# Performance work log

Measured on AMD Instinct MI355X. Metric: run time of the kernel, lower is better.

The kernel has to match this reference:

```python
import jax, jax.numpy as jnp
import numpy as np

BS = 128
HW = 128
REG = 0.1


def setup_inputs() -> dict:
    key = jax.random.key(0)
    k1, k2 = jax.random.split(key)
    x1 = jax.random.normal(k1, (BS, 1, HW, HW), dtype=jnp.float32)
    x2 = jax.random.normal(k2, (BS, 1, HW, HW), dtype=jnp.float32)
    return {"x1": x1, "x2": x2}


def _calc_psd(x):
    # x: [2*bs, H, W]
    dft = jnp.fft.fft2(x)
    avgpsd = jnp.mean((dft * jnp.conj(dft)).real, axis=0)  # [H, W]
    return jnp.mean(jnp.log(avgpsd)) - jnp.log(jnp.mean(avgpsd))


def reference(x1, x2):
    a = x1[:, 0]  # [bs, H, W] (squeeze channel)
    b = x2[:, 0]
    # pairwise Frobenius distances: Dist[i, j] = ||x1[i] - x2[j]||_F
    diff = a[:, None, :, :] - b[None, :, :, :]          # [bs, bs, H, W]
    Dist = jnp.sqrt(jnp.sum(diff * diff, axis=(-2, -1)))  # [bs, bs]
    bs = Dist.shape[0]
    # CrossEntropyLoss(Dist, arange(bs)) = mean_i(logsumexp(Dist[i]) - Dist[i, i])
    log_probs = jax.nn.log_softmax(Dist, axis=-1)
    ce = -jnp.mean(jnp.diagonal(log_probs))
    # PSD regularizer on cat(x1, x2)
    x = jnp.concatenate([a, b], axis=0)  # [2*bs, H, W]
    r = _calc_psd(x)
    return ce - REG * r
```

## Files before the change

### kernel.cpp

```cpp
#include <hip/hip_runtime.h>
#include <math.h>


#define WS_SE    256
#define WS_MX    512
#define WS_DII   768
#define WS_NP    16640
#define WS_GP    20736
#define WS_P     4215040
#define WS_PS    6344960
#define WS_PL    6345025

#define PI_F 3.14159265358979323846f

__device__ __forceinline__ void fft128_reg(float& s0r, float& s0i,
                                           float& s1r, float& s1i,
                                           float cA, float sA,
                                           const float* wr, const float* wi,
                                           int lane) {
    float er = s0r + s1r, ei = s0i + s1i;
    float dr = s0r - s1r, di = s0i - s1i;
    float orr = dr * cA - di * sA;
    float oii = dr * sA + di * cA;
    #pragma unroll
    for (int st = 0; st < 6; ++st) {
        int m = 32 >> st;
        bool up = (lane & m) == 0;
        float tr = __shfl_xor(er, m), ti = __shfl_xor(ei, m);
        float ar = tr - er, ai = ti - ei;
        float e2r = up ? (er + tr) : (ar * wr[st] - ai * wi[st]);
        float e2i = up ? (ei + ti) : (ar * wi[st] + ai * wr[st]);
        tr = __shfl_xor(orr, m); ti = __shfl_xor(oii, m);
        float br_ = tr - orr, bi_ = ti - oii;
        float o2r = up ? (orr + tr) : (br_ * wr[st] - bi_ * wi[st]);
        float o2i = up ? (oii + ti) : (br_ * wi[st] + bi_ * wr[st]);
        er = e2r; ei = e2i; orr = o2r; oii = o2i;
    }
    s0r = er; s0i = ei; s1r = orr; s1i = oii;
}

__global__ __launch_bounds__(512, 4) void ocl_main(const float* __restrict__ x1,
                                                   const float* __restrict__ x2,
                                                   float* __restrict__ ws) {
    __shared__ float4 smem4[4096];
    int t = threadIdx.x;
    int bid = blockIdx.x;

    if (bid < 256) {
        float4* As = smem4;
        float4* Bs = smem4 + 2048;
        int ks = bid, k0q = ks * 16;
        const float4* A = (const float4*)x1;
        const float4* B = (const float4*)x2;
        {
            int qi = t & 15, r0 = t >> 4;
            #pragma unroll
            for (int p = 0; p < 4; ++p) {
                int r = r0 + 32 * p;
                int sq = qi ^ ((r >> 3) & 7);
                As[r * 16 + sq] = A[(size_t)r * 4096 + k0q + qi];
                Bs[r * 16 + sq] = B[(size_t)r * 4096 + k0q + qi];
            }
        }
        __syncthreads();
        if (t >= 256) return;

        int ty = t >> 4, tx = t & 15;
        float acc[8][8];
        #pragma unroll
        for (int r = 0; r < 8; ++r)
            #pragma unroll
            for (int c = 0; c < 8; ++c) acc[r][c] = 0.0f;

        for (int qk = 0; qk < 16; ++qk) {
            int sa = qk ^ (ty & 7);
            int sb = qk ^ (tx & 7);
            float4 a4[8];
            #pragma unroll
            for (int r = 0; r < 8; ++r) a4[r] = As[(ty * 8 + r) * 16 + sa];
            #pragma unroll
            for (int h = 0; h < 2; ++h) {
                float4 b4[4];
                #pragma unroll
                for (int c = 0; c < 4; ++c)
                    b4[c] = Bs[(tx * 8 + h * 4 + c) * 16 + sb];
                #pragma unroll
                for (int r = 0; r < 8; ++r)
                    #pragma unroll
                    for (int c = 0; c < 4; ++c) {
                        float4 a = a4[r], b = b4[c];
                        acc[r][h * 4 + c] = fmaf(a.x, b.x, fmaf(a.y, b.y,
                            fmaf(a.z, b.z, fmaf(a.w, b.w, acc[r][h * 4 + c]))));
                    }
            }
        }

        float4* Gp4 = (float4*)(ws + WS_GP);
        #pragma unroll
        for (int r = 0; r < 8; ++r)
            #pragma unroll
            for (int cc = 0; cc < 2; ++cc) {
                int e4 = (ty * 8 + r) * 32 + tx * 2 + cc;
                Gp4[(size_t)(e4 >> 2) * 1024 + ks * 4 + (e4 & 3)] =
                    make_float4(acc[r][cc * 4 + 0], acc[r][cc * 4 + 1],
                                acc[r][cc * 4 + 2], acc[r][cc * 4 + 3]);
            }
    } else {
        float* zre = (float*)smem4;
        float* zim = zre + 8192;
        int lane = t & 63, wave = t >> 6;
        int img = bid - 256;
        const float* src = (img < 128) ? (x1 + (size_t)img * 16384)
                                       : (x2 + (size_t)(img - 128) * 16384);

        float cA, sA, wr[6], wi[6];
        {
            float th = -PI_F * (float)lane / 64.0f;
            sA = __sinf(th); cA = __cosf(th);
            #pragma unroll
            for (int st = 0; st < 6; ++st) {
                int m = 32 >> st;
                float a = -PI_F * (float)(lane & (m - 1)) / (float)m;
                wi[st] = __sinf(a); wr[st] = __cosf(a);
            }
        }
        int rb = (int)(__brev((unsigned)lane) >> 26);

        float nrm = 0.0f;
        #pragma unroll
        for (int pi = 0; pi < 8; ++pi) {
            int p = wave * 8 + pi;
            const float* r0 = src + p * 256 + lane;
            float s0r = r0[0],   s1r = r0[64];
            float s0i = r0[128], s1i = r0[192];
            nrm += s0r * s0r + s1r * s1r + s0i * s0i + s1i * s1i;
            fft128_reg(s0r, s0i, s1r, s1i, cA, sA, wr, wi, lane);
            int f0 = (2 * rb + p) & 127;
            int f1 = (2 * rb + 1 + p) & 127;
            zre[p * 128 + f0] = s0r; zim[p * 128 + f0] = s0i;
            zre[p * 128 + f1] = s1r; zim[p * 128 + f1] = s1i;
        }
        for (int off = 32; off >= 1; off >>= 1) nrm += __shfl_xor(nrm, off);
        if (lane == 0) ws[WS_NP + img * 8 + wave] = nrm;
        __syncthreads();

        int p0 = (lane >> 1), p1 = 32 + (lane >> 1);
        int par = lane & 1;
        float* P = ws + WS_P;
        for (int k = wave; k < 65; k += 8) {
            float v0r, v0i, v1r, v1i;
            if (k == 0 || k == 64) {
                int c0 = (k + p0) & 127, c1 = (k + p1) & 127;
                float Z0r = zre[p0 * 128 + c0], Z0i = zim[p0 * 128 + c0];
                float Z1r = zre[p1 * 128 + c1], Z1i = zim[p1 * 128 + c1];
                v0r = par ? Z0i : Z0r; v0i = 0.0f;
                v1r = par ? Z1i : Z1r; v1i = 0.0f;
            } else {
                int kn = 128 - k;
                int ck = (k + p0) & 127, cn = (kn + p0) & 127;
                float Zkr = zre[p0 * 128 + ck], Zki = zim[p0 * 128 + ck];
                float Znr = zre[p0 * 128 + cn], Zni = zim[p0 * 128 + cn];
                float e0r = 0.5f * (Zkr + Znr), e0i = 0.5f * (Zki - Zni);
                float q0r = 0.5f * (Zki + Zni), q0i = 0.5f * (Znr - Zkr);
                v0r = par ? q0r : e0r; v0i = par ? q0i : e0i;
                ck = (k + p1) & 127; cn = (kn + p1) & 127;
                Zkr = zre[p1 * 128 + ck]; Zki = zim[p1 * 128 + ck];
                Znr = zre[p1 * 128 + cn]; Zni = zim[p1 * 128 + cn];
                float e1r = 0.5f * (Zkr + Znr), e1i = 0.5f * (Zki - Zni);
                float q1r = 0.5f * (Zki + Zni), q1i = 0.5f * (Znr - Zkr);
                v1r = par ? q1r : e1r; v1i = par ? q1i : e1i;
            }
            fft128_reg(v0r, v0i, v1r, v1i, cA, sA, wr, wi, lane);
            int m = lane & 15, hi = lane >> 4;
            P[(size_t)(k * 8 + 0 + hi) * 4096 + img * 16 + m] = v0r * v0r + v0i * v0i;
            P[(size_t)(k * 8 + 4 + hi) * 4096 + img * 16 + m] = v1r * v1r + v1i * v1i;
        }
    }
}

__global__ __launch_bounds__(256) void ocl_finish(float* __restrict__ ws) {
    int bid = blockIdx.x, t = threadIdx.x;
    int lane = t & 63, wave = t >> 6;

    if (bid < 256) {
        int g = bid;
        const float4* Gp4 = (const float4*)(ws + WS_GP);
        int q = (lane >> 4) & 3, kg = lane & 15;
        const float4* base = Gp4 + (size_t)g * 4096 + wave * 1024 + q;
        float4 v[16];
        #pragma unroll
        for (int it = 0; it < 16; ++it) v[it] = base[(kg * 16 + it) * 4];

        __shared__ float nbs[64];
        __shared__ float s_na;
        __shared__ float sm[4], sm2[4];
        if (t < 64) {
            const float* np = ws + WS_NP + (size_t)(128 + (g & 1) * 64 + t) * 8;
            nbs[t] = ((np[0] + np[1]) + (np[2] + np[3])) +
                     ((np[4] + np[5]) + (np[6] + np[7]));
        }
        if (t == 64) {
            const float* np = ws + WS_NP + (size_t)(g >> 1) * 8;
            s_na = ((np[0] + np[1]) + (np[2] + np[3])) +
                   ((np[4] + np[5]) + (np[6] + np[7]));
        }

        float4 s = v[0];
        #pragma unroll
        for (int it = 1; it < 16; ++it) {
            s.x += v[it].x; s.y += v[it].y; s.z += v[it].z; s.w += v[it].w;
        }
        #pragma unroll
        for (int msk = 1; msk <= 8; msk <<= 1) {
            s.x += __shfl_xor(s.x, msk); s.y += __shfl_xor(s.y, msk);
            s.z += __shfl_xor(s.z, msk); s.w += __shfl_xor(s.w, msk);
        }
        __syncthreads();

        int cq = wave * 4 + q;
        float nai = s_na;
        float4 d;
        d.x = sqrtf(fmaxf(nai + nbs[cq * 4 + 0] - 2.0f * s.x, 0.0f));
        d.y = sqrtf(fmaxf(nai + nbs[cq * 4 + 1] - 2.0f * s.y, 0.0f));
        d.z = sqrtf(fmaxf(nai + nbs[cq * 4 + 2] - 2.0f * s.z, 0.0f));
        d.w = sqrtf(fmaxf(nai + nbs[cq * 4 + 3] - 2.0f * s.w, 0.0f));

        int i = g >> 1;
        int jr = i - (g & 1) * 64;
        if (kg == 0 && jr >= 0 && jr < 64 && cq == (jr >> 2)) {
            float dii = (jr & 2) ? ((jr & 1) ? d.w : d.z) : ((jr & 1) ? d.y : d.x);
            ws[WS_DII + i] = dii;
        }

        float m = fmaxf(fmaxf(d.x, d.y), fmaxf(d.z, d.w));
        m = fmaxf(m, __shfl_xor(m, 16));
        m = fmaxf(m, __shfl_xor(m, 32));
        if (lane == 0) sm[wave] = m;
        __syncthreads();
        float M = fmaxf(fmaxf(sm[0], sm[1]), fmaxf(sm[2], sm[3]));

        float se = __expf(d.x - M) + __expf(d.y - M) +
                   __expf(d.z - M) + __expf(d.w - M);
        se += __shfl_xor(se, 16);
        se += __shfl_xor(se, 32);
        if (lane == 0) sm2[wave] = se;
        __syncthreads();
        if (t == 0) {
            ws[WS_SE + g] = sm2[0] + sm2[1] + sm2[2] + sm2[3];
            ws[WS_MX + g] = M;
        }
    } else {
        int k = bid - 256;
        const float4* P4 = (const float4*)(ws + WS_P);
        int b16 = t >> 5, m4 = (t >> 3) & 3, hq = t & 7;
        const float4* base = P4 + (size_t)(k * 8 + b16) * 1024 + m4;
        float4 s = make_float4(0.f, 0.f, 0.f, 0.f);
        #pragma unroll
        for (int half = 0; half < 2; ++half) {
            float4 u[16];
            #pragma unroll
            for (int it = 0; it < 16; ++it)
                u[it] = base[(hq * 32 + half * 16 + it) * 4];
            #pragma unroll
            for (int it = 0; it < 16; ++it) {
                s.x += u[it].x; s.y += u[it].y; s.z += u[it].z; s.w += u[it].w;
            }
        }
        #pragma unroll
        for (int msk = 1; msk <= 4; msk <<= 1) {
            s.x += __shfl_xor(s.x, msk); s.y += __shfl_xor(s.y, msk);
            s.z += __shfl_xor(s.z, msk); s.w += __shfl_xor(s.w, msk);
        }
        float sS = 0.0f, sL = 0.0f;
        if (hq == 0) {
            float w = (k == 0 || k == 64) ? 1.0f : 2.0f;
            sS = w * (s.x + s.y + s.z + s.w);
            sL = w * (logf(s.x) + logf(s.y) + logf(s.z) + logf(s.w));
        }
        #pragma unroll
        for (int off = 32; off >= 1; off >>= 1) {
            sS += __shfl_xor(sS, off);
            sL += __shfl_xor(sL, off);
        }
        __shared__ float aS[4], aL[4];
        if (lane == 0) { aS[wave] = sS; aL[wave] = sL; }
        __syncthreads();
        if (t == 0) {
            ws[WS_PS + k] = aS[0] + aS[1] + aS[2] + aS[3];
            ws[WS_PL + k] = aL[0] + aL[1] + aL[2] + aL[3];
        }
    }
}

__global__ __launch_bounds__(256) void ocl_tail(const float* __restrict__ ws,
                                                float* __restrict__ out) {
    int t = threadIdx.x, lane = t & 63, wave = t >> 6;

    float rowacc = 0.0f;
    if (t < 128) {
        int i = t;
        float sea = ws[WS_SE + 2 * i],     seb = ws[WS_SE + 2 * i + 1];
        float ma  = ws[WS_MX + 2 * i],     mb  = ws[WS_MX + 2 * i + 1];
        float dii = ws[WS_DII + i];
        float M = fmaxf(ma, mb);
        float se = sea * __expf(ma - M) + seb * __expf(mb - M);
        rowacc = M + logf(se) - dii;
    }

    float sS = 0.0f, sL = 0.0f;
    if (t < 65) { sS = ws[WS_PS + t]; sL = ws[WS_PL + t]; }
    #pragma unroll
    for (int off = 32; off >= 1; off >>= 1) {
        sS += __shfl_xor(sS, off);
        sL += __shfl_xor(sL, off);
        rowacc += __shfl_xor(rowacc, off);
    }
    __shared__ float bS[4], bL[4], bR[4];
    if (lane == 0) { bS[wave] = sS; bL[wave] = sL; bR[wave] = rowacc; }
    __syncthreads();
    if (t == 0) {
        float S_ = bS[0] + bS[1] + bS[2] + bS[3];
        float L_ = bL[0] + bL[1] + bL[2] + bL[3];
        float R_ = bR[0] + bR[1] + bR[2] + bR[3];
        float ce = R_ / 128.0f;
        float r  = L_ / 16384.0f - logf(S_ / 16384.0f);
        out[0] = ce - 0.1f * r;
    }
}

extern "C" void kernel_launch(void* const* d_in, const int* in_sizes, int n_in,
                              void* d_out, int out_size, void* d_ws, size_t ws_size,
                              hipStream_t stream) {
    (void)in_sizes; (void)n_in; (void)out_size; (void)ws_size;
    const float* x1 = (const float*)d_in[0];
    const float* x2 = (const float*)d_in[1];
    float* ws  = (float*)d_ws;
    float* out = (float*)d_out;

    hipLaunchKernelGGL(ocl_main,   dim3(512), dim3(512), 0, stream, x1, x2, ws);
    hipLaunchKernelGGL(ocl_finish, dim3(321), dim3(256), 0, stream, ws);
    hipLaunchKernelGGL(ocl_tail,   dim3(1),   dim3(256), 0, stream, ws, out);
}
```

Baseline: 94.97 us.

## Use DPP for small FFT butterflies and read A tiles directly from global

The FFT butterfly stages with xor distance 2 and 1 now use DPP quad-permute moves instead of generic shuffles, which are meant to be cheaper than ds_bpermute-style exchanges. In the Gram kernel, the A operand is no longer staged in LDS. Each thread loads its 8 A rows straight from global memory through cache, while only B stays in shared memory. This halves LDS usage and drops one staging step, but it adds global-load latency inside the inner loop.

```diff
diff --git a/kernel.cpp b/kernel.cpp
--- a/kernel.cpp
+++ b/kernel.cpp
@@ -12,6 +12,17 @@
 #define WS_PL    6345025
 
 #define PI_F 3.14159265358979323846f
+
+#define SHX32(v) __shfl_xor((v), 32)
+#define SHX16(v) __shfl_xor((v), 16)
+#define SHX8(v)  __shfl_xor((v), 8)
+#define SHX4(v)  __shfl_xor((v), 4)
+__device__ __forceinline__ float DPPX2(float v) {
+    return __int_as_float(__builtin_amdgcn_mov_dpp(__float_as_int(v), 0x4E, 0xf, 0xf, true));
+}
+__device__ __forceinline__ float DPPX1(float v) {
+    return __int_as_float(__builtin_amdgcn_mov_dpp(__float_as_int(v), 0xB1, 0xf, 0xf, true));
+}
 
 __device__ __forceinline__ void fft128_reg(float& s0r, float& s0i,
                                            float& s1r, float& s1i,
@@ -22,20 +33,24 @@
     float dr = s0r - s1r, di = s0i - s1i;
     float orr = dr * cA - di * sA;
     float oii = dr * sA + di * cA;
-    #pragma unroll
-    for (int st = 0; st < 6; ++st) {
-        int m = 32 >> st;
-        bool up = (lane & m) == 0;
-        float tr = __shfl_xor(er, m), ti = __shfl_xor(ei, m);
-        float ar = tr - er, ai = ti - ei;
-        float e2r = up ? (er + tr) : (ar * wr[st] - ai * wi[st]);
-        float e2i = up ? (ei + ti) : (ar * wi[st] + ai * wr[st]);
-        tr = __shfl_xor(orr, m); ti = __shfl_xor(oii, m);
-        float br_ = tr - orr, bi_ = ti - oii;
-        float o2r = up ? (orr + tr) : (br_ * wr[st] - bi_ * wi[st]);
-        float o2i = up ? (oii + ti) : (br_ * wi[st] + bi_ * wr[st]);
-        er = e2r; ei = e2i; orr = o2r; oii = o2i;
-    }
+#define OCL_ST(ST, M, EXCH)                                           \
+    { bool up = (lane & (M)) == 0;                                    \
+      float tr = EXCH(er), ti = EXCH(ei);                             \
+      float ar = tr - er, ai = ti - ei;                               \
+      float e2r = up ? (er + tr) : (ar * wr[ST] - ai * wi[ST]);       \
+      float e2i = up ? (ei + ti) : (ar * wi[ST] + ai * wr[ST]);       \
+      tr = EXCH(orr); ti = EXCH(oii);                                 \
+      float br_ = tr - orr, bi_ = ti - oii;                           \
+      float o2r = up ? (orr + tr) : (br_ * wr[ST] - bi_ * wi[ST]);    \
+      float o2i = up ? (oii + ti) : (br_ * wi[ST] + bi_ * wr[ST]);    \
+      er = e2r; ei = e2i; orr = o2r; oii = o2i; }
+    OCL_ST(0, 32, SHX32)
+    OCL_ST(1, 16, SHX16)
+    OCL_ST(2, 8,  SHX8)
+    OCL_ST(3, 4,  SHX4)
+    OCL_ST(4, 2,  DPPX2)
+    OCL_ST(5, 1,  DPPX1)
+#undef OCL_ST
     s0r = er; s0i = ei; s1r = orr; s1i = oii;
 }
 
@@ -47,8 +62,7 @@
     int bid = blockIdx.x;
 
     if (bid < 256) {
-        float4* As = smem4;
-        float4* Bs = smem4 + 2048;
+        float4* Bs = smem4;
         int ks = bid, k0q = ks * 16;
         const float4* A = (const float4*)x1;
         const float4* B = (const float4*)x2;
@@ -58,7 +72,6 @@
             for (int p = 0; p < 4; ++p) {
                 int r = r0 + 32 * p;
                 int sq = qi ^ ((r >> 3) & 7);
-                As[r * 16 + sq] = A[(size_t)r * 4096 + k0q + qi];
                 Bs[r * 16 + sq] = B[(size_t)r * 4096 + k0q + qi];
             }
         }
@@ -66,6 +79,7 @@
         if (t >= 256) return;
 
         int ty = t >> 4, tx = t & 15;
+        const float4* Arow = A + (size_t)(ty * 8) * 4096 + k0q;
         float acc[8][8];
         #pragma unroll
         for (int r = 0; r < 8; ++r)
@@ -73,24 +87,24 @@
             for (int c = 0; c < 8; ++c) acc[r][c] = 0.0f;
 
         for (int qk = 0; qk < 16; ++qk) {
-            int sa = qk ^ (ty & 7);
             int sb = qk ^ (tx & 7);
-            float4 a4[8];
-            #pragma unroll
-            for (int r = 0; r < 8; ++r) a4[r] = As[(ty * 8 + r) * 16 + sa];
-            #pragma unroll
-            for (int h = 0; h < 2; ++h) {
-                float4 b4[4];
+            float4 b4[8];
+            #pragma unroll
+            for (int c = 0; c < 8; ++c)
+                b4[c] = Bs[(tx * 8 + c) * 16 + sb];
+            #pragma unroll
+            for (int rh = 0; rh < 2; ++rh) {
+                float4 a4[4];
                 #pragma unroll
-                for (int c = 0; c < 4; ++c)
-                    b4[c] = Bs[(tx * 8 + h * 4 + c) * 16 + sb];
+                for (int r = 0; r < 4; ++r)
+                    a4[r] = Arow[(size_t)(rh * 4 + r) * 4096 + qk];
                 #pragma unroll
-                for (int r = 0; r < 8; ++r)
+                for (int r = 0; r < 4; ++r)
                     #pragma unroll
-                    for (int c = 0; c < 4; ++c) {
+                    for (int c = 0; c < 8; ++c) {
                         float4 a = a4[r], b = b4[c];
-                        acc[r][h * 4 + c] = fmaf(a.x, b.x, fmaf(a.y, b.y,
-                            fmaf(a.z, b.z, fmaf(a.w, b.w, acc[r][h * 4 + c]))));
+                        acc[rh * 4 + r][c] = fmaf(a.x, b.x, fmaf(a.y, b.y,
+                            fmaf(a.z, b.z, fmaf(a.w, b.w, acc[rh * 4 + r][c]))));
                     }
             }
         }
```

New measurement: 91.77 us. 3.4% less time.
